# Kernel optimization log

Measured on AMD Instinct MI355X. Metric: run time of the kernel, lower is better.

## Reference

```python
import jax, jax.numpy as jnp
import numpy as np

B, S, D = 2, 2048, 1024
E, K = 8, 2
CAP_FACTOR = 1.25
HID = 4 * D


def _capacity(num_tokens: int) -> int:
    import math
    cap = math.floor(K * CAP_FACTOR * num_tokens / E)
    cap += cap % 2
    return max(int(cap), 2)


def setup_inputs() -> dict:
    key = jax.random.key(0)
    k1, k2, k3, k4 = jax.random.split(key, 4)
    x = jax.random.normal(k1, (B, S, D), dtype=jnp.float32)
    w_gate = jax.random.normal(k2, (D, E), dtype=jnp.float32) * 0.02
    w_fc = jax.random.normal(k3, (E, D, HID), dtype=jnp.float32) * 0.02
    w_proj = jax.random.normal(k4, (E, HID, D), dtype=jnp.float32) * 0.02
    return {"x": x, "w_gate": w_gate, "w_fc": w_fc, "w_proj": w_proj}


def _moe_forward(x, w_gate, w_fc, w_proj):
    b, s, d = x.shape
    T = b * s
    cap = _capacity(T)
    xf = x.astype(jnp.float32).reshape(T, d)

    # --- Router (fp32, eval mode: no noise) ---
    logits = xf @ w_gate                                   # [T, E]
    top_v, top_i = jax.lax.top_k(logits, K)                # [T, K]
    NEG = jnp.float32(-1e30)
    masked = jnp.full_like(logits, NEG)
    masked = masked.at[jnp.arange(T)[:, None], top_i].set(top_v)
    probs = jax.nn.softmax(masked, axis=-1)                # [T, E], zero off top-k

    # --- Capacity assignment: cumsum over (k-major, token) flattened order ---
    oh = jax.nn.one_hot(top_i, E, dtype=jnp.int32)         # [T, K, E]
    oh = jnp.transpose(oh, (1, 0, 2))                      # [K, T, E]
    rank = jnp.cumsum(oh.reshape(K * T, E), axis=0).reshape(K, T, E) - 1
    within = (oh > 0) & (rank < cap)                       # [K, T, E]
    rank_sel = jnp.sum(jnp.where(within, rank, 0), axis=-1)  # [K, T]
    kept = jnp.any(within, axis=-1)                        # [K, T]

    p = jnp.take_along_axis(probs, top_i, axis=-1).T       # [K, T]
    w = jnp.where(kept, p, 0.0)                            # combine weights

    e_idx = top_i.T                                        # [K, T]
    t_idx = jnp.broadcast_to(jnp.arange(T)[None, :], (K, T))

    # expert_weights[t, e, c] (sparse scatter == torch one-hot combine)
    expert_weights = jnp.zeros((T, E, cap), jnp.float32)
    expert_weights = expert_weights.at[t_idx.ravel(), e_idx.ravel(), rank_sel.ravel()].add(w.ravel())

    # dispatch: expert_batches[e, c, :] = x of token routed to (e, c)
    disp = jnp.where(kept, 1.0, 0.0).ravel()[:, None]      # [K*T, 1]
    expert_batches = jnp.zeros((E, cap, d), jnp.float32)
    expert_batches = expert_batches.at[e_idx.ravel(), rank_sel.ravel()].add(disp * xf[t_idx.ravel()])

    # --- Expert MLPs (batched GEMMs, exact GELU, no bias, eval dropout) ---
    h = jnp.einsum('ecd,edh->ech', expert_batches, w_fc)
    h = jax.nn.gelu(h, approximate=False)
    expert_out = jnp.einsum('ech,ehd->ecd', h, w_proj)      # [E, cap, d]

    # --- Combine: gather expert outputs back to tokens weighted by router prob ---
    gathered = expert_out[e_idx.ravel(), rank_sel.ravel()].reshape(K, T, d)
    out_flat = jnp.sum(w[:, :, None] * gathered, axis=0)    # [T, d]
    output = out_flat.reshape(b, s, d)

    # --- Load balance loss (Switch) ---
    probs_full = jax.nn.softmax(logits, axis=-1)
    prob_per_expert = jnp.mean(probs_full, axis=0)          # [E]
    tokens_per_expert = jax.lax.stop_gradient(
        jnp.sum((expert_weights > 0).astype(jnp.float32), axis=(0, 2)) / (T * K)
    )
    lb_loss = E * jnp.sum(prob_per_expert * tokens_per_expert)

    # --- Router z-loss ---
    z_loss = jnp.mean(jax.nn.logsumexp(logits, axis=-1) ** 2)
    return output, lb_loss, z_loss


def reference(x, w_gate, w_fc, w_proj):
    return _moe_forward(x, w_gate, w_fc, w_proj)
```

## Files before the change

### kernel.cpp

```cpp
#include <hip/hip_runtime.h>
#include <hip/hip_bf16.h>
#include <cstdint>
#include <cstddef>

#define T_TOK 4096
#define D_DIM 1024
#define E_EXP 8
#define KSEL 2
#define CAP 1280
#define HID_DIM 4096

typedef __attribute__((ext_vector_type(8))) __bf16 bf16x8;
typedef __attribute__((ext_vector_type(8))) unsigned short ushort8;
typedef __attribute__((ext_vector_type(4))) float floatx4;

__device__ __forceinline__ unsigned short f2bf(float f) {
  unsigned int u = __builtin_bit_cast(unsigned int, f);
  u = (u + 0x7FFFu + ((u >> 16) & 1u)) >> 16;
  return (unsigned short)u;
}
__device__ __forceinline__ float bf2f(unsigned short h) {
  unsigned int u = ((unsigned int)h) << 16;
  return __builtin_bit_cast(float, u);
}

__device__ __forceinline__ void async16(const unsigned short* g, unsigned short* l) {
  __builtin_amdgcn_global_load_lds(
      (const __attribute__((address_space(1))) unsigned int*)g,
      (__attribute__((address_space(3))) unsigned int*)l, 16, 0, 0);
}

__global__ void router_kernel(const float* __restrict__ x, const float* __restrict__ wg,
                              int* __restrict__ top1, int* __restrict__ top2,
                              float* __restrict__ p0, float* __restrict__ p1,
                              float* __restrict__ probsum, float* __restrict__ zsum) {
  __shared__ float lps[E_EXP];
  __shared__ float lz;
  if (threadIdx.x < E_EXP) lps[threadIdx.x] = 0.f;
  if (threadIdx.x == 0) lz = 0.f;
  __syncthreads();
  int wave = threadIdx.x >> 6;
  int lane = threadIdx.x & 63;
  int t = blockIdx.x * 4 + wave;
  const float* xr = x + (size_t)t * D_DIM;
  float acc[E_EXP];
#pragma unroll
  for (int e = 0; e < E_EXP; ++e) acc[e] = 0.f;
  for (int j = 0; j < D_DIM / 64; ++j) {
    int i = lane + 64 * j;
    float xv = xr[i];
    const float4* wr = (const float4*)(wg + (size_t)i * E_EXP);
    float4 w0 = wr[0], w1 = wr[1];
    acc[0] += xv * w0.x; acc[1] += xv * w0.y; acc[2] += xv * w0.z; acc[3] += xv * w0.w;
    acc[4] += xv * w1.x; acc[5] += xv * w1.y; acc[6] += xv * w1.z; acc[7] += xv * w1.w;
  }
#pragma unroll
  for (int e = 0; e < E_EXP; ++e) {
#pragma unroll
    for (int s = 32; s > 0; s >>= 1) acc[e] += __shfl_xor(acc[e], s);
  }
  if (lane == 0) {
    int i1 = 0; float v1 = acc[0];
    for (int e = 1; e < E_EXP; ++e) if (acc[e] > v1) { v1 = acc[e]; i1 = e; }
    int i2 = -1; float v2 = -1e30f;
    for (int e = 0; e < E_EXP; ++e) if (e != i1 && acc[e] > v2) { v2 = acc[e]; i2 = e; }
    top1[t] = i1; top2[t] = i2;
    float dexp = expf(v2 - v1);
    p0[t] = 1.f / (1.f + dexp);
    p1[t] = dexp / (1.f + dexp);
    float pe[E_EXP]; float ssum = 0.f;
    for (int e = 0; e < E_EXP; ++e) { pe[e] = expf(acc[e] - v1); ssum += pe[e]; }
    float lse = logf(ssum) + v1;
    atomicAdd(&lz, lse * lse);
    float inv = 1.f / ssum;
    for (int e = 0; e < E_EXP; ++e) atomicAdd(&lps[e], pe[e] * inv);
  }
  __syncthreads();
  if (threadIdx.x < E_EXP) atomicAdd(&probsum[threadIdx.x], lps[threadIdx.x]);
  if (threadIdx.x == 0) atomicAdd(zsum, lz);
}

__global__ void scan_kernel(const int* __restrict__ top1, const int* __restrict__ top2,
                            int* __restrict__ rank0, int* __restrict__ rank1,
                            int* __restrict__ slot_token, int* __restrict__ cntk) {
  __shared__ int sc[256][E_EXP];
  int c = threadIdx.x;
  int e0l[16], e1l[16];
  int c0[E_EXP], c1[E_EXP];
#pragma unroll
  for (int e = 0; e < E_EXP; ++e) { c0[e] = 0; c1[e] = 0; }
#pragma unroll
  for (int j = 0; j < 16; ++j) {
    int t = c * 16 + j;
    int a = top1[t]; int b = top2[t];
    e0l[j] = a; e1l[j] = b;
    c0[a]++; c1[b]++;
  }
  for (int e = 0; e < E_EXP; ++e) sc[c][e] = c0[e];
  __syncthreads();
  for (int s = 1; s < 256; s <<= 1) {
    int tmp[E_EXP];
    if (c >= s) { for (int e = 0; e < E_EXP; ++e) tmp[e] = sc[c - s][e]; }
    __syncthreads();
    if (c >= s) { for (int e = 0; e < E_EXP; ++e) sc[c][e] += tmp[e]; }
    __syncthreads();
  }
  int off0[E_EXP], tot0[E_EXP];
  for (int e = 0; e < E_EXP; ++e) {
    off0[e] = (c > 0) ? sc[c - 1][e] : 0;
    tot0[e] = sc[255][e];
  }
  __syncthreads();
  for (int e = 0; e < E_EXP; ++e) sc[c][e] = c1[e];
  __syncthreads();
  for (int s = 1; s < 256; s <<= 1) {
    int tmp[E_EXP];
    if (c >= s) { for (int e = 0; e < E_EXP; ++e) tmp[e] = sc[c - s][e]; }
    __syncthreads();
    if (c >= s) { for (int e = 0; e < E_EXP; ++e) sc[c][e] += tmp[e]; }
    __syncthreads();
  }
  int off1[E_EXP], tot1[E_EXP];
  for (int e = 0; e < E_EXP; ++e) {
    off1[e] = (c > 0) ? sc[c - 1][e] : 0;
    tot1[e] = sc[255][e];
  }
  int run[E_EXP];
  for (int e = 0; e < E_EXP; ++e) run[e] = off0[e];
#pragma unroll
  for (int j = 0; j < 16; ++j) {
    int t = c * 16 + j;
    int e = e0l[j];
    int r = run[e]++;
    if (r < CAP) { rank0[t] = r; slot_token[e * CAP + r] = t; } else rank0[t] = -1;
  }
  for (int e = 0; e < E_EXP; ++e) run[e] = tot0[e] + off1[e];
#pragma unroll
  for (int j = 0; j < 16; ++j) {
    int t = c * 16 + j;
    int e = e1l[j];
    int r = run[e]++;
    if (r < CAP) { rank1[t] = r; slot_token[e * CAP + r] = t; } else rank1[t] = -1;
  }
  if (c == 0) {
    for (int e = 0; e < E_EXP; ++e) {
      int tot = tot0[e] + tot1[e];
      cntk[e] = tot < CAP ? tot : CAP;
    }
  }
}

__global__ void dispatch_kernel(const float* __restrict__ x, const int* __restrict__ slot_token,
                                unsigned short* __restrict__ batch) {
  int slot = blockIdx.x;
  int t = slot_token[slot];
  int d = threadIdx.x * 4;
  ushort4 o;
  if (t >= 0) {
    float4 v = *(const float4*)(x + (size_t)t * D_DIM + d);
    o.x = f2bf(v.x); o.y = f2bf(v.y); o.z = f2bf(v.z); o.w = f2bf(v.w);
  } else {
    o.x = 0; o.y = 0; o.z = 0; o.w = 0;
  }
  *(ushort4*)(batch + (size_t)slot * D_DIM + d) = o;
}

__global__ __launch_bounds__(256) void transpose_convert(const float* __restrict__ in,
                                                         unsigned short* __restrict__ out,
                                                         int R, int C) {
  __shared__ float tile[64][65];
  int b = blockIdx.z;
  int c0 = blockIdx.x * 64;
  int r0 = blockIdx.y * 64;
  const float* ip = in + (size_t)b * R * C;
  unsigned short* op = out + (size_t)b * R * C;
  int tid = threadIdx.x;
  int rr = tid >> 4;
  int cc = (tid & 15) * 4;
#pragma unroll
  for (int it = 0; it < 4; ++it) {
    int r = rr + it * 16;
    float4 v = *(const float4*)(ip + (size_t)(r0 + r) * C + c0 + cc);
    tile[r][cc] = v.x; tile[r][cc + 1] = v.y; tile[r][cc + 2] = v.z; tile[r][cc + 3] = v.w;
  }
  __syncthreads();
  int c = tid >> 2;
  int rq = (tid & 3) * 16;
  unsigned short vals[16];
#pragma unroll
  for (int j = 0; j < 16; ++j) vals[j] = f2bf(tile[rq + j][c]);
  unsigned short* dst = op + (size_t)(c0 + c) * R + r0 + rq;
  *(ushort8*)dst = *(ushort8*)&vals[0];
  *(ushort8*)(dst + 8) = *(ushort8*)&vals[8];
}

template <int KD, int NN, int NG_TILES, bool GELU>
__global__ __launch_bounds__(256) void gemm_alds(const unsigned short* __restrict__ A,
                                                 const unsigned short* __restrict__ BT,
                                                 unsigned short* __restrict__ Cd,
                                                 const int* __restrict__ cntk) {
  constexpr int MT = CAP / 128;
  constexpr int GRP = MT * NG_TILES;
  int bid = blockIdx.x;
  int e = bid & 7;
  int slot = bid >> 3;
  int ng = slot / GRP;
  int rem = slot - ng * GRP;
  int mm = rem / NG_TILES;
  int nw = rem - mm * NG_TILES;
  int m0 = mm * 128;
  int n0 = (ng * NG_TILES + nw) * 128;
  if (m0 >= cntk[e]) return;
  const unsigned short* Ae = A + (size_t)e * CAP * KD;
  const unsigned short* Be = BT + (size_t)e * NN * KD;
  unsigned short* Ce = Cd + (size_t)e * CAP * NN;
  __shared__ unsigned short As[128 * 32];
  __shared__ unsigned short Bs[128 * 32];
  int tid = threadIdx.x;
  int lane = tid & 63;
  int wv = tid >> 6;
  int wm = (wv & 1) * 64;
  int wn = (wv >> 1) * 64;
  int mrow = lane & 15;
  int kqb = lane >> 4;
  int sx = (mrow >> 1) & 3;
  int kb = (kqb ^ sx) * 8;
  floatx4 acc[4][4];
#pragma unroll
  for (int i = 0; i < 4; ++i)
#pragma unroll
    for (int j = 0; j < 4; ++j) {
      floatx4 z = {0.f, 0.f, 0.f, 0.f};
      acc[i][j] = z;
    }
  for (int k0 = 0; k0 < KD; k0 += 32) {
#pragma unroll
    for (int i = 0; i < 2; ++i) {
      int chw = i * 256 + wv * 64;
      int ch = chw + lane;
      int r = ch >> 2;
      int cbs = (ch & 3) ^ ((r >> 1) & 3);
      async16(&Ae[(size_t)(m0 + r) * KD + k0 + cbs * 8], &As[chw * 8]);
      async16(&Be[(size_t)(n0 + r) * KD + k0 + cbs * 8], &Bs[chw * 8]);
    }
    __syncthreads();
    bf16x8 af[4], bfr[4];
#pragma unroll
    for (int mt = 0; mt < 4; ++mt)
      af[mt] = *(const bf16x8*)(&As[(wm + mt * 16 + mrow) * 32 + kb]);
#pragma unroll
    for (int nt = 0; nt < 4; ++nt)
      bfr[nt] = *(const bf16x8*)(&Bs[(wn + nt * 16 + mrow) * 32 + kb]);
#pragma unroll
    for (int mt = 0; mt < 4; ++mt)
#pragma unroll
      for (int nt = 0; nt < 4; ++nt)
        acc[mt][nt] = __builtin_amdgcn_mfma_f32_16x16x32_bf16(af[mt], bfr[nt], acc[mt][nt], 0, 0, 0);
    __syncthreads();
  }
  int crow = (lane >> 4) * 4;
  int ccol = lane & 15;
#pragma unroll
  for (int mt = 0; mt < 4; ++mt)
#pragma unroll
    for (int nt = 0; nt < 4; ++nt)
#pragma unroll
      for (int r = 0; r < 4; ++r) {
        float v = acc[mt][nt][r];
        if (GELU) v = 0.5f * v * (1.f + erff(v * 0.70710678118654752f));
        Ce[(size_t)(m0 + wm + mt * 16 + crow + r) * NN + (n0 + wn + nt * 16 + ccol)] = f2bf(v);
      }
}

__global__ void combine_kernel(const unsigned short* __restrict__ EO,
                               const int* __restrict__ top1, const int* __restrict__ top2,
                               const float* __restrict__ p0, const float* __restrict__ p1,
                               const int* __restrict__ rank0, const int* __restrict__ rank1,
                               float* __restrict__ out) {
  int t = blockIdx.x;
  int d = threadIdx.x * 4;
  float a0 = 0.f, a1 = 0.f, a2 = 0.f, a3 = 0.f;
  int r0 = rank0[t];
  if (r0 >= 0) {
    float w = p0[t];
    ushort4 v = *(const ushort4*)(EO + ((size_t)top1[t] * CAP + r0) * D_DIM + d);
    a0 += w * bf2f(v.x); a1 += w * bf2f(v.y); a2 += w * bf2f(v.z); a3 += w * bf2f(v.w);
  }
  int r1 = rank1[t];
  if (r1 >= 0) {
    float w = p1[t];
    ushort4 v = *(const ushort4*)(EO + ((size_t)top2[t] * CAP + r1) * D_DIM + d);
    a0 += w * bf2f(v.x); a1 += w * bf2f(v.y); a2 += w * bf2f(v.z); a3 += w * bf2f(v.w);
  }
  float4 o; o.x = a0; o.y = a1; o.z = a2; o.w = a3;
  *(float4*)(out + (size_t)t * D_DIM + d) = o;
}

__global__ void finalize_kernel(const float* __restrict__ probsum, const float* __restrict__ zsum,
                                const int* __restrict__ cntk, float* __restrict__ out) {
  if (threadIdx.x == 0) {
    float lb = 0.f;
    for (int e = 0; e < E_EXP; ++e)
      lb += (probsum[e] / (float)T_TOK) * ((float)cntk[e] / (float)(T_TOK * KSEL));
    out[(size_t)T_TOK * D_DIM] = lb * (float)E_EXP;
    out[(size_t)T_TOK * D_DIM + 1] = zsum[0] / (float)T_TOK;
  }
}

extern "C" void kernel_launch(void* const* d_in, const int* in_sizes, int n_in,
                              void* d_out, int out_size, void* d_ws, size_t ws_size,
                              hipStream_t stream) {
  const float* x = (const float*)d_in[0];
  const float* w_gate = (const float*)d_in[1];
  const float* w_fc = (const float*)d_in[2];
  const float* w_proj = (const float*)d_in[3];
  float* out = (float*)d_out;
  char* ws = (char*)d_ws;

  float* probsum = (float*)(ws + 0);
  float* zsum    = (float*)(ws + 32);
  int*   cntk    = (int*)(ws + 64);
  int*   top1    = (int*)(ws + 4096);
  int*   top2    = (int*)(ws + 20480);
  float* p0      = (float*)(ws + 36864);
  float* p1      = (float*)(ws + 53248);
  int*   rank0   = (int*)(ws + 69632);
  int*   rank1   = (int*)(ws + 86016);
  int*   slot    = (int*)(ws + 102400);
  unsigned short* batch = (unsigned short*)(ws + 262144);
  unsigned short* H     = (unsigned short*)(ws + 262144 + 20971520);
  unsigned short* EO    = (unsigned short*)(ws + 262144 + 20971520 + 83886080);
  unsigned short* W     = (unsigned short*)(ws + 262144 + 20971520 + 83886080 + 20971520);

  hipMemsetAsync(ws, 0, 4096, stream);
  hipMemsetAsync(slot, 0xFF, E_EXP * CAP * sizeof(int), stream);

  router_kernel<<<T_TOK / 4, 256, 0, stream>>>(x, w_gate, top1, top2, p0, p1, probsum, zsum);
  scan_kernel<<<1, 256, 0, stream>>>(top1, top2, rank0, rank1, slot, cntk);
  dispatch_kernel<<<E_EXP * CAP, 256, 0, stream>>>(x, slot, batch);

  transpose_convert<<<dim3(HID_DIM / 64, D_DIM / 64, E_EXP), 256, 0, stream>>>(w_fc, W, D_DIM, HID_DIM);
  gemm_alds<D_DIM, HID_DIM, 4, true><<<8 * (HID_DIM / 128 / 4) * (CAP / 128) * 4, 256, 0, stream>>>(batch, W, H, cntk);

  transpose_convert<<<dim3(D_DIM / 64, HID_DIM / 64, E_EXP), 256, 0, stream>>>(w_proj, W, HID_DIM, D_DIM);
  gemm_alds<HID_DIM, D_DIM, 2, false><<<8 * (D_DIM / 128 / 2) * (CAP / 128) * 2, 256, 0, stream>>>(H, W, EO, cntk);

  combine_kernel<<<T_TOK, 256, 0, stream>>>(EO, top1, top2, p0, p1, rank0, rank1, out);
  finalize_kernel<<<1, 64, 0, stream>>>(probsum, zsum, cntk, out);
}
```

Measured before the change: 584.1 us.

## Double GEMM K-tile to 64, convert-then-transpose weights in LDS, fuse finalize

The GEMM K step grows from 32 to 64. Each barrier pair now covers two MFMA sub-steps, and the LDS swizzle changes to an 8-way XOR for the 128-byte rows. This halves the synchronisation and loop overhead per unit of work, at the cost of twice the LDS per block, which can lower occupancy. The weight transpose now converts to bf16 before staging in LDS, so the tile is half the size and reads are vectorised. The separate finalize kernel is folded into the combine kernel to save one launch.

```diff
diff --git a/kernel.cpp b/kernel.cpp
--- a/kernel.cpp
+++ b/kernel.cpp
@@ -12,6 +12,7 @@
 
 typedef __attribute__((ext_vector_type(8))) __bf16 bf16x8;
 typedef __attribute__((ext_vector_type(8))) unsigned short ushort8;
+typedef __attribute__((ext_vector_type(4))) unsigned short ushort4v;
 typedef __attribute__((ext_vector_type(4))) float floatx4;
 
 __device__ __forceinline__ unsigned short f2bf(float f) {
@@ -168,30 +169,32 @@
 __global__ __launch_bounds__(256) void transpose_convert(const float* __restrict__ in,
                                                          unsigned short* __restrict__ out,
                                                          int R, int C) {
-  __shared__ float tile[64][65];
+  __shared__ unsigned short tl[64 * 72];
   int b = blockIdx.z;
   int c0 = blockIdx.x * 64;
   int r0 = blockIdx.y * 64;
   const float* ip = in + (size_t)b * R * C;
   unsigned short* op = out + (size_t)b * R * C;
   int tid = threadIdx.x;
-  int rr = tid >> 4;
-  int cc = (tid & 15) * 4;
-#pragma unroll
-  for (int it = 0; it < 4; ++it) {
-    int r = rr + it * 16;
-    float4 v = *(const float4*)(ip + (size_t)(r0 + r) * C + c0 + cc);
-    tile[r][cc] = v.x; tile[r][cc + 1] = v.y; tile[r][cc + 2] = v.z; tile[r][cc + 3] = v.w;
-  }
-  __syncthreads();
-  int c = tid >> 2;
-  int rq = (tid & 3) * 16;
-  unsigned short vals[16];
-#pragma unroll
-  for (int j = 0; j < 16; ++j) vals[j] = f2bf(tile[rq + j][c]);
-  unsigned short* dst = op + (size_t)(c0 + c) * R + r0 + rq;
-  *(ushort8*)dst = *(ushort8*)&vals[0];
-  *(ushort8*)(dst + 8) = *(ushort8*)&vals[8];
+  int mr = tid >> 4;
+  int mc = tid & 15;
+  unsigned short q[4][4];
+#pragma unroll
+  for (int j = 0; j < 4; ++j) {
+    float4 v = *(const float4*)(ip + (size_t)(r0 + mr * 4 + j) * C + c0 + mc * 4);
+    q[0][j] = f2bf(v.x); q[1][j] = f2bf(v.y); q[2][j] = f2bf(v.z); q[3][j] = f2bf(v.w);
+  }
+#pragma unroll
+  for (int j = 0; j < 4; ++j)
+    *(ushort4v*)(&tl[(mc * 4 + j) * 72 + mr * 4]) = *(ushort4v*)&q[j][0];
+  __syncthreads();
+  int row = tid >> 2;
+  int seg = (tid & 3) * 16;
+  ushort8 a = *(const ushort8*)(&tl[row * 72 + seg]);
+  ushort8 bb = *(const ushort8*)(&tl[row * 72 + seg + 8]);
+  unsigned short* dst = op + (size_t)(c0 + row) * R + r0 + seg;
+  *(ushort8*)dst = a;
+  *(ushort8*)(dst + 8) = bb;
 }
 
 template <int KD, int NN, int NG_TILES, bool GELU>
@@ -214,8 +217,8 @@
   const unsigned short* Ae = A + (size_t)e * CAP * KD;
   const unsigned short* Be = BT + (size_t)e * NN * KD;
   unsigned short* Ce = Cd + (size_t)e * CAP * NN;
-  __shared__ unsigned short As[128 * 32];
-  __shared__ unsigned short Bs[128 * 32];
+  __shared__ unsigned short As[128 * 64];
+  __shared__ unsigned short Bs[128 * 64];
   int tid = threadIdx.x;
   int lane = tid & 63;
   int wv = tid >> 6;
@@ -223,8 +226,6 @@
   int wn = (wv >> 1) * 64;
   int mrow = lane & 15;
   int kqb = lane >> 4;
-  int sx = (mrow >> 1) & 3;
-  int kb = (kqb ^ sx) * 8;
   floatx4 acc[4][4];
 #pragma unroll
   for (int i = 0; i < 4; ++i)
@@ -233,29 +234,33 @@
       floatx4 z = {0.f, 0.f, 0.f, 0.f};
       acc[i][j] = z;
     }
-  for (int k0 = 0; k0 < KD; k0 += 32) {
-#pragma unroll
-    for (int i = 0; i < 2; ++i) {
+  for (int k0 = 0; k0 < KD; k0 += 64) {
+#pragma unroll
+    for (int i = 0; i < 4; ++i) {
       int chw = i * 256 + wv * 64;
       int ch = chw + lane;
-      int r = ch >> 2;
-      int cbs = (ch & 3) ^ ((r >> 1) & 3);
-      async16(&Ae[(size_t)(m0 + r) * KD + k0 + cbs * 8], &As[chw * 8]);
-      async16(&Be[(size_t)(n0 + r) * KD + k0 + cbs * 8], &Bs[chw * 8]);
+      int r = ch >> 3;
+      int gb = (ch & 7) ^ (r & 7);
+      async16(&Ae[(size_t)(m0 + r) * KD + k0 + gb * 8], &As[chw * 8]);
+      async16(&Be[(size_t)(n0 + r) * KD + k0 + gb * 8], &Bs[chw * 8]);
     }
     __syncthreads();
-    bf16x8 af[4], bfr[4];
-#pragma unroll
-    for (int mt = 0; mt < 4; ++mt)
-      af[mt] = *(const bf16x8*)(&As[(wm + mt * 16 + mrow) * 32 + kb]);
-#pragma unroll
-    for (int nt = 0; nt < 4; ++nt)
-      bfr[nt] = *(const bf16x8*)(&Bs[(wn + nt * 16 + mrow) * 32 + kb]);
-#pragma unroll
-    for (int mt = 0; mt < 4; ++mt)
+#pragma unroll
+    for (int kh = 0; kh < 2; ++kh) {
+      int posA = ((kh * 4 + kqb) ^ (mrow & 7)) * 8;
+      bf16x8 af[4], bfr[4];
+#pragma unroll
+      for (int mt = 0; mt < 4; ++mt)
+        af[mt] = *(const bf16x8*)(&As[(wm + mt * 16 + mrow) * 64 + posA]);
 #pragma unroll
       for (int nt = 0; nt < 4; ++nt)
-        acc[mt][nt] = __builtin_amdgcn_mfma_f32_16x16x32_bf16(af[mt], bfr[nt], acc[mt][nt], 0, 0, 0);
+        bfr[nt] = *(const bf16x8*)(&Bs[(wn + nt * 16 + mrow) * 64 + posA]);
+#pragma unroll
+      for (int mt = 0; mt < 4; ++mt)
+#pragma unroll
+        for (int nt = 0; nt < 4; ++nt)
+          acc[mt][nt] = __builtin_amdgcn_mfma_f32_16x16x32_bf16(af[mt], bfr[nt], acc[mt][nt], 0, 0, 0);
+    }
     __syncthreads();
   }
   int crow = (lane >> 4) * 4;
@@ -276,7 +281,8 @@
                                const int* __restrict__ top1, const int* __restrict__ top2,
                                const float* __restrict__ p0, const float* __restrict__ p1,
                                const int* __restrict__ rank0, const int* __restrict__ rank1,
-                               float* __restrict__ out) {
+                               const float* __restrict__ probsum, const float* __restrict__ zsum,
+                               const int* __restrict__ cntk, float* __restrict__ out) {
   int t = blockIdx.x;
   int d = threadIdx.x * 4;
   float a0 = 0.f, a1 = 0.f, a2 = 0.f, a3 = 0.f;
@@ -294,11 +300,7 @@
   }
   float4 o; o.x = a0; o.y = a1; o.z = a2; o.w = a3;
   *(float4*)(out + (size_t)t * D_DIM + d) = o;
-}
-
-__global__ void finalize_kernel(const float* __restrict__ probsum, const float* __restrict__ zsum,
-                                const int* __restrict__ cntk, float* __restrict__ out) {
-  if (threadIdx.x == 0) {
+  if (t == 0 && threadIdx.x == 0) {
     float lb = 0.f;
     for (int e = 0; e < E_EXP; ++e)
       lb += (probsum[e] / (float)T_TOK) * ((float)cntk[e] / (float)(T_TOK * KSEL));
@@ -345,6 +347,6 @@
   transpose_convert<<<dim3(D_DIM / 64, HID_DIM / 64, E_EXP), 256, 0, stream>>>(w_proj, W, HID_DIM, D_DIM);
   gemm_alds<HID_DIM, D_DIM, 2, false><<<8 * (D_DIM / 128 / 2) * (CAP / 128) * 2, 256, 0, stream>>>(H, W, EO, cntk);
 
-  combine_kernel<<<T_TOK, 256, 0, stream>>>(EO, top1, top2, p0, p1, rank0, rank1, out);
-  finalize_kernel<<<1, 64, 0, stream>>>(probsum, zsum, cntk, out);
-}
+  combine_kernel<<<T_TOK, 256, 0, stream>>>(EO, top1, top2, p0, p1, rank0, rank1,
+                                            probsum, zsum, cntk, out);
+}
```

Measured after the change: 602.9 us. 1.03x slower.
